# Optimization experiments

Hardware: AMD Instinct MI355X
Metric: run time of the kernel (lower is better)

## Reference

```python
import jax, jax.numpy as jnp
import numpy as np

HEADS = 12
LN_EPS = 1e-12
NUM_PROTOTYPES = 8


def _layer_norm(x, g, b):
    mu = x.mean(-1, keepdims=True)
    var = ((x - mu) ** 2).mean(-1, keepdims=True)
    return (x - mu) / jnp.sqrt(var + LN_EPS) * g + b


def _bert_attention(q_in, kv_in, wq, bq, wk, bk, wv, bv, wo, bo, ln_g, ln_b):
    # HF BertAttention: MHA (query from q_in, key/value from kv_in) then
    # SelfOutput: dense + residual(q_in) + LayerNorm. Dropout = 0 (eval).
    B, Sq, D = q_in.shape
    Sk = kv_in.shape[1]
    dh = D // HEADS
    q = (q_in @ wq + bq).reshape(B, Sq, HEADS, dh).transpose(0, 2, 1, 3)
    k = (kv_in @ wk + bk).reshape(B, Sk, HEADS, dh).transpose(0, 2, 1, 3)
    v = (kv_in @ wv + bv).reshape(B, Sk, HEADS, dh).transpose(0, 2, 1, 3)
    scores = jnp.einsum('bhqd,bhkd->bhqk', q, k) / jnp.sqrt(jnp.asarray(dh, q.dtype))
    probs = jax.nn.softmax(scores, axis=-1)
    ctx = jnp.einsum('bhqk,bhkd->bhqd', probs, v).transpose(0, 2, 1, 3).reshape(B, Sq, D)
    return _layer_norm(ctx @ wo + bo + q_in, ln_g, ln_b)


def setup_inputs() -> dict:
    key = jax.random.key(0)
    ks = jax.random.split(key, 16)
    D = 768
    inp = {
        'local_feats': jax.random.normal(ks[0], (8, 256, D), jnp.float32),
        'global_feat_dict': jax.random.normal(ks[1], (16384, D), jnp.float32),
    }
    i = 2
    for pre in ('ll', 'lg'):
        for nm in ('wq', 'wk', 'wv', 'wo'):
            inp[f'{pre}_{nm}'] = 0.02 * jax.random.normal(ks[i], (D, D), jnp.float32)
            i += 1
        for nm in ('bq', 'bk', 'bv', 'bo'):
            inp[f'{pre}_{nm}'] = jnp.zeros((D,), jnp.float32)
        inp[f'{pre}_ln_g'] = jnp.ones((D,), jnp.float32)
        inp[f'{pre}_ln_b'] = jnp.zeros((D,), jnp.float32)
    inp['ln_g'] = jnp.ones((D,), jnp.float32)
    inp['ln_b'] = jnp.zeros((D,), jnp.float32)
    inp['aug_w'] = 0.02 * jax.random.normal(ks[i], (D, 1), jnp.float32)
    inp['ori_w'] = 0.02 * jax.random.normal(ks[i + 1], (D, 1), jnp.float32)
    inp['aug_b'] = jnp.zeros((1,), jnp.float32)
    inp['ori_b'] = jnp.zeros((1,), jnp.float32)
    return inp


def reference(local_feats, global_feat_dict,
              ll_wq, ll_bq, ll_wk, ll_bk, ll_wv, ll_bv, ll_wo, ll_bo, ll_ln_g, ll_ln_b,
              lg_wq, lg_bq, lg_wk, lg_bk, lg_wv, lg_bv, lg_wo, lg_bo, lg_ln_g, lg_ln_b,
              ln_g, ln_b, aug_w, aug_b, ori_w, ori_b):
    B, L, D = local_feats.shape
    K = NUM_PROTOTYPES
    # similarity_topk retrieval: cosine similarity against prototype pool
    g_norm = global_feat_dict / jnp.linalg.norm(global_feat_dict, axis=-1, keepdims=True)
    t_norm = local_feats / jnp.linalg.norm(local_feats, axis=-1, keepdims=True)
    sim = jnp.einsum('bld,nd->bln', t_norm, g_norm)          # [B, L, N]
    topk_idx = jax.lax.top_k(sim, K)[1]                       # [B, L, K]
    global_feats = global_feat_dict[topk_idx].reshape(B, L * K, D)
    # self-attn over locals, cross-attn locals -> retrieved prototypes
    ll = _bert_attention(local_feats, local_feats,
                         ll_wq, ll_bq, ll_wk, ll_bk, ll_wv, ll_bv, ll_wo, ll_bo, ll_ln_g, ll_ln_b)
    lg = _bert_attention(local_feats, global_feats,
                         lg_wq, lg_bq, lg_wk, lg_bk, lg_wv, lg_bv, lg_wo, lg_bo, lg_ln_g, lg_ln_b)
    out = _layer_norm(ll + lg, ln_g, ln_b)
    aug_weight = jax.nn.sigmoid(out @ aug_w + aug_b + local_feats @ ori_w + ori_b)
    return aug_weight * out + (1.0 - aug_weight) * local_feats
```

## Files before the change

### kernel.cpp

```cpp
#include <hip/hip_runtime.h>
#include <math.h>

#define D     768
#define HEADS 12
#define DH    64
#define BATCH 8
#define LSEQ  256
#define MROWS 2048
#define NDICT 16384
#define TOPK  8

typedef _Float16 half_t;
typedef half_t half8 __attribute__((ext_vector_type(8)));
typedef float floatx4 __attribute__((ext_vector_type(4)));

#define F_DICT   0u
#define F_TN     6291456u
#define F_LOC    7077888u
#define F_WT     7864320u
#define F_BF     10223616u
#define F_TOPI   10231808u
#define F_LP     10248192u
#define F_SIM    13393920u
#define F_CTX    30171136u
#define F_D1     30957568u
#define F_CANDV  30957568u
#define F_CANDI  31088640u
#define F_ML     34103296u
#define F_NRM    34299904u
#define F_USED   34316288u
#define F_ROWMAP 34332672u
#define F_INVMAP 34349056u
#define F_CNT    34365440u

typedef const __attribute__((address_space(1))) void* gptr_as1;
typedef __attribute__((address_space(3))) void* lptr_as3;
#define GLDS16(gp, lp) __builtin_amdgcn_global_load_lds((gptr_as1)(gp), (lptr_as3)(lp), 16, 0, 0)

__device__ __forceinline__ float bsum(float v, float* red) {
  int t = threadIdx.x;
#pragma unroll
  for (int d = 32; d > 0; d >>= 1) v += __shfl_xor(v, d);
  if ((t & 63) == 0) red[t >> 6] = v;
  __syncthreads();
  float r = red[0] + red[1] + red[2] + red[3];
  __syncthreads();
  return r;
}

__global__ __launch_bounds__(256) void k_prep_wt(
    const float* __restrict__ dict, const float* __restrict__ local,
    half_t* __restrict__ gdict_h, float* __restrict__ dnrm,
    half_t* __restrict__ loc_h, half_t* __restrict__ tn_h,
    const float* w0, const float* w1, const float* w2, const float* w3,
    const float* w4, const float* w5, const float* w6, const float* w7,
    const float* b0, const float* b1, const float* b2, const float* b3,
    const float* b4, const float* b5, const float* b6, const float* b7,
    half_t* __restrict__ Wt, float* __restrict__ bfout) {
  __shared__ float red[8];
  __shared__ float tile[32][33];
  int g = blockIdx.x, t = threadIdx.x;
  if (g < NDICT) {
    const float* xr = dict + (size_t)g * D;
    float v0 = xr[t], v1 = xr[t + 256], v2 = xr[t + 512];
    float s = bsum(v0*v0 + v1*v1 + v2*v2, red);
    float n = sqrtf(s), inv = 1.0f / n;
    half_t* yr = gdict_h + (size_t)g * D;
    yr[t] = (half_t)(v0*inv); yr[t+256] = (half_t)(v1*inv); yr[t+512] = (half_t)(v2*inv);
    if (t == 0) dnrm[g] = n;
  } else if (g < NDICT + MROWS) {
    size_t r = g - NDICT;
    const float* xr = local + r * (size_t)D;
    float v0 = xr[t], v1 = xr[t + 256], v2 = xr[t + 512];
    float s = bsum(v0*v0 + v1*v1 + v2*v2, red);
    float inv = 1.0f / sqrtf(s);
    half_t* rr = loc_h + r * (size_t)D;
    half_t* nr = tn_h + r * (size_t)D;
    rr[t] = (half_t)v0;        rr[t+256] = (half_t)v1;        rr[t+512] = (half_t)v2;
    nr[t] = (half_t)(v0*inv);  nr[t+256] = (half_t)(v1*inv);  nr[t+512] = (half_t)(v2*inv);
  } else {
    const float* wsrcs[8] = {w0,w1,w2,w3,w4,w5,w6,w7};
    const float* bsrcs[8] = {b0,b1,b2,b3,b4,b5,b6,b7};
    int id = g - (NDICT + MROWS);
    int z = id / 576, rem = id % 576;
    int by = rem / 24, bx = rem % 24;
    const float* Wsrc = wsrcs[z];
    half_t* dst = Wt + (size_t)z * D * D;
    int tx = t & 31, ty = t >> 5;
    int c0 = bx * 32, r0 = by * 32;
#pragma unroll
    for (int j = 0; j < 4; j++)
      tile[ty + j*8][tx] = Wsrc[(size_t)(r0 + ty + j*8) * D + c0 + tx];
    __syncthreads();
#pragma unroll
    for (int j = 0; j < 4; j++)
      dst[(size_t)(c0 + ty + j*8) * D + r0 + tx] = (half_t)tile[tx][ty + j*8];
    if (bx == 0 && by == 0) {
#pragma unroll
      for (int j = 0; j < 3; j++)
        bfout[z * D + t + j*256] = bsrcs[z][t + j*256];
    }
  }
}

__device__ __forceinline__ void hgemm_core(
    const half_t* __restrict__ A, const half_t* __restrict__ B,
    const float* __restrict__ bias, const float* __restrict__ dnrm,
    const int* __restrict__ rowmap, void* __restrict__ Cout,
    int N, int K, int outHalf, int bx, int by, int mhalf,
    half_t* As, half_t* Bs) {
  int tid = threadIdx.x;
  int wid = tid >> 6, lane = tid & 63;
  int l16 = lane & 15, quad = lane >> 4;
  int n0 = bx * 128, m0 = by * 128;
  if (mhalf && m0 >= mhalf) { B += (size_t)D * D; if (bias) bias += D; }
  int wm = (wid & 1) * 64, wn = (wid >> 1) * 64;

  int r0  = tid >> 3;
  int cbg = (tid & 7) ^ (r0 & 7);
  const half_t* Aps[4];
#pragma unroll
  for (int i = 0; i < 4; i++) {
    int mm = m0 + r0 + 32*i;
    int mr = rowmap ? rowmap[mm] : mm;
    Aps[i] = A + (size_t)mr * K + cbg * 8;
  }
  const half_t* Bp = B + (size_t)(n0 + r0) * K + cbg * 8;

  floatx4 acc[4][4];
#pragma unroll
  for (int i = 0; i < 4; i++)
#pragma unroll
    for (int j = 0; j < 4; j++) { acc[i][j][0]=0.f; acc[i][j][1]=0.f; acc[i][j][2]=0.f; acc[i][j][3]=0.f; }

  for (int k0 = 0; k0 < K; k0 += 64) {
#pragma unroll
    for (int i = 0; i < 4; i++)
      GLDS16(Aps[i] + k0, As + ((size_t)i*256 + wid*64) * 8);
#pragma unroll
    for (int i = 0; i < 4; i++)
      GLDS16(Bp + k0 + (size_t)i * 32 * K, Bs + ((size_t)i*256 + wid*64) * 8);
    __syncthreads();
#pragma unroll
    for (int ks = 0; ks < 2; ks++) {
      half8 af[4], bf[4];
#pragma unroll
      for (int i = 0; i < 4; i++) {
        int row = wm + i*16 + l16;
        int cb = (quad + ks*4) ^ (row & 7);
        af[i] = *(const half8*)&As[row*64 + cb*8];
      }
#pragma unroll
      for (int j = 0; j < 4; j++) {
        int row = wn + j*16 + l16;
        int cb = (quad + ks*4) ^ (row & 7);
        bf[j] = *(const half8*)&Bs[row*64 + cb*8];
      }
#pragma unroll
      for (int i = 0; i < 4; i++)
#pragma unroll
        for (int j = 0; j < 4; j++)
          acc[i][j] = __builtin_amdgcn_mfma_f32_16x16x32_f16(af[i], bf[j], acc[i][j], 0, 0, 0);
    }
    __syncthreads();
  }

  float bcol[4];
#pragma unroll
  for (int j = 0; j < 4; j++) bcol[j] = bias ? bias[n0 + wn + j*16 + l16] : 0.f;
  if (outHalf) {
    half_t* C = (half_t*)Cout;
#pragma unroll
    for (int i = 0; i < 4; i++)
#pragma unroll
      for (int r = 0; r < 4; r++) {
        int grow = m0 + wm + i*16 + quad*4 + r;
        float sc = dnrm ? dnrm[rowmap ? rowmap[grow] : grow] : 1.0f;
#pragma unroll
        for (int j = 0; j < 4; j++)
          C[(size_t)grow * N + n0 + wn + j*16 + l16] = (half_t)(acc[i][j][r] * sc + bcol[j]);
      }
  } else {
    float* C = (float*)Cout;
#pragma unroll
    for (int i = 0; i < 4; i++)
#pragma unroll
      for (int r = 0; r < 4; r++) {
        int grow = m0 + wm + i*16 + quad*4 + r;
        float sc = dnrm ? dnrm[rowmap ? rowmap[grow] : grow] : 1.0f;
#pragma unroll
        for (int j = 0; j < 4; j++)
          C[(size_t)grow * N + n0 + wn + j*16 + l16] = acc[i][j][r] * sc + bcol[j];
      }
  }
}

__device__ __forceinline__ void hgemm256_core(
    const half_t* __restrict__ A, const half_t* __restrict__ B,
    const float* __restrict__ bias, const float* __restrict__ dnrm,
    const int* __restrict__ rowmap, half_t* __restrict__ C,
    int N, int K, int bx, int by,
    half_t* As0, half_t* As1, half_t* Bs0, half_t* Bs1) {
  const int tid = threadIdx.x;
  const int wid = tid >> 6, lane = tid & 63;
  const int l16 = lane & 15, quad = lane >> 4;
  const int m0 = by * 256, n0 = bx * 256;

  const int r0 = tid >> 3;
  const int cg = (tid & 7) ^ (r0 & 7);
  const half_t* Aps[4]; const half_t* Bps[4];
#pragma unroll
  for (int i = 0; i < 4; i++) {
    int mm = m0 + r0 + i * 64;
    int mr = rowmap ? rowmap[mm] : mm;
    Aps[i] = A + (size_t)mr * K + cg * 8;
    Bps[i] = B + (size_t)(n0 + r0 + i * 64) * K + cg * 8;
  }

  const int arow = (wid & 3) * 32 + l16;
  const int brow = (wid >> 2) * 64 + l16;
  const int cb0 = (quad ^ (l16 & 7)) * 8;
  const int cb1 = ((quad + 4) ^ (l16 & 7)) * 8;

  floatx4 acc[4][2][4];
#pragma unroll
  for (int q = 0; q < 4; q++)
#pragma unroll
    for (int mi = 0; mi < 2; mi++)
#pragma unroll
      for (int ni = 0; ni < 4; ni++) {
        acc[q][mi][ni][0] = 0.f; acc[q][mi][ni][1] = 0.f;
        acc[q][mi][ni][2] = 0.f; acc[q][mi][ni][3] = 0.f;
      }
  half8 af[2][2], bf[4][2];

#define STAGE(Adst, Bdst, kn) { \
    GLDS16(Aps[0] + (kn), (Adst) + (0*512 + wid*64) * 8); \
    GLDS16(Aps[1] + (kn), (Adst) + (1*512 + wid*64) * 8); \
    GLDS16(Aps[2] + (kn), (Adst) + (2*512 + wid*64) * 8); \
    GLDS16(Aps[3] + (kn), (Adst) + (3*512 + wid*64) * 8); \
    GLDS16(Bps[0] + (kn), (Bdst) + (0*512 + wid*64) * 8); \
    GLDS16(Bps[1] + (kn), (Bdst) + (1*512 + wid*64) * 8); \
    GLDS16(Bps[2] + (kn), (Bdst) + (2*512 + wid*64) * 8); \
    GLDS16(Bps[3] + (kn), (Bdst) + (3*512 + wid*64) * 8); }
#define LDA(qm) { const int rb_ = (qm)*8192 + arow*64; \
    af[0][0] = *(const half8*)&Ar[rb_ + cb0];        af[0][1] = *(const half8*)&Ar[rb_ + cb1]; \
    af[1][0] = *(const half8*)&Ar[rb_ + 1024 + cb0]; af[1][1] = *(const half8*)&Ar[rb_ + 1024 + cb1]; }
#define LDB(qn) { const int rb_ = (qn)*8192 + brow*64; \
    bf[0][0] = *(const half8*)&Br[rb_ + cb0];        bf[0][1] = *(const half8*)&Br[rb_ + cb1]; \
    bf[1][0] = *(const half8*)&Br[rb_ + 1024 + cb0]; bf[1][1] = *(const half8*)&Br[rb_ + 1024 + cb1]; \
    bf[2][0] = *(const half8*)&Br[rb_ + 2048 + cb0]; bf[2][1] = *(const half8*)&Br[rb_ + 2048 + cb1]; \
    bf[3][0] = *(const half8*)&Br[rb_ + 3072 + cb0]; bf[3][1] = *(const half8*)&Br[rb_ + 3072 + cb1]; }
#define MM(q) { _Pragma("unroll") for (int mi = 0; mi < 2; mi++) { \
    _Pragma("unroll") for (int ni = 0; ni < 4; ni++) { \
      acc[q][mi][ni] = __builtin_amdgcn_mfma_f32_16x16x32_f16(af[mi][0], bf[ni][0], acc[q][mi][ni], 0, 0, 0); \
      acc[q][mi][ni] = __builtin_amdgcn_mfma_f32_16x16x32_f16(af[mi][1], bf[ni][1], acc[q][mi][ni], 0, 0, 0); } } }

  const int NT = K >> 6;
  STAGE(As0, Bs0, 0);
  __syncthreads();

  half_t* Ar = As0; half_t* Aw = As1;
  half_t* Br = Bs0; half_t* Bw = Bs1;
  for (int t = 0; t < NT; ++t) {
    if (t + 1 < NT) STAGE(Aw, Bw, (t + 1) * 64);
    LDA(0); LDB(0); MM(0);
    LDB(1);         MM(1);
    LDA(1);         MM(2);
    LDB(0);         MM(3);
    if (t + 1 < NT) __syncthreads();
    half_t* tp = Ar; Ar = Aw; Aw = tp;
    tp = Br; Br = Bw; Bw = tp;
  }

  float bcol[2][4];
#pragma unroll
  for (int qn = 0; qn < 2; qn++)
#pragma unroll
    for (int ni = 0; ni < 4; ni++)
      bcol[qn][ni] = bias ? bias[n0 + qn*128 + (wid >> 2)*64 + ni*16 + l16] : 0.f;
#pragma unroll
  for (int q = 0; q < 4; q++) {
    const int qm = q >> 1;
    const int qn = (q == 1 || q == 2) ? 1 : 0;
#pragma unroll
    for (int mi = 0; mi < 2; mi++)
#pragma unroll
      for (int r = 0; r < 4; r++) {
        int grow = m0 + qm*128 + (wid & 3)*32 + mi*16 + quad*4 + r;
        float sc = dnrm ? dnrm[rowmap ? rowmap[grow] : grow] : 1.0f;
#pragma unroll
        for (int ni = 0; ni < 4; ni++)
          C[(size_t)grow * N + n0 + qn*128 + (wid >> 2)*64 + ni*16 + l16] =
              (half_t)(acc[q][mi][ni][r] * sc + bcol[qn][ni]);
      }
  }
#undef STAGE
#undef LDA
#undef LDB
#undef MM
}

__global__ __launch_bounds__(512) void k_gemm_simlp(
    const half_t* __restrict__ tn, const half_t* __restrict__ gd,
    half_t* __restrict__ sim,
    const half_t* __restrict__ loc, const half_t* __restrict__ wt0,
    const float* __restrict__ bf0, half_t* __restrict__ lp) {
  __shared__ half_t As[2][256*64];
  __shared__ half_t Bs[2][256*64];
  int gid = blockIdx.x;
  int swz = (gid & 7) * 76 + (gid >> 3);
  if (swz < 512) {
    int bx = (swz & 7) + ((swz >> 3) >> 3) * 8;
    int by = (swz >> 3) & 7;
    hgemm256_core(tn, gd, nullptr, nullptr, nullptr, sim, NDICT, D, bx, by,
                  As[0], As[1], Bs[0], Bs[1]);
  } else {
    int rel = swz - 512;
    int bx = rel >> 3;
    int by = rel & 7;
    hgemm256_core(loc, wt0, bf0, nullptr, nullptr, lp, 3072, D, bx, by,
                  As[0], As[1], Bs[0], Bs[1]);
  }
}

__global__ __launch_bounds__(512) void k_gemm_dkv(
    const half_t* __restrict__ gd, const half_t* __restrict__ wt4,
    const float* __restrict__ bf4, const float* __restrict__ dnrm,
    const int* __restrict__ rowmap, const int* __restrict__ cnt,
    half_t* __restrict__ dkv) {
  __shared__ half_t As[2][256*64];
  __shared__ half_t Bs[2][256*64];
  int mceil = (*cnt + 255) & ~255;
  if ((int)blockIdx.y * 256 >= mceil) return;
  hgemm256_core(gd, wt4, bf4, dnrm, rowmap, dkv, 1536, D,
                blockIdx.x, blockIdx.y, As[0], As[1], Bs[0], Bs[1]);
}

__global__ __launch_bounds__(256) void k_gemm_wo(
    const half_t* __restrict__ ctx, const half_t* __restrict__ wt6,
    const float* __restrict__ bf6, float* __restrict__ dd) {
  __shared__ half_t As[128*64];
  __shared__ half_t Bs[128*64];
  hgemm_core(ctx, wt6, bf6, nullptr, nullptr, dd, D, D, 0, blockIdx.x, blockIdx.y, MROWS, As, Bs);
}

__global__ __launch_bounds__(256) void k_topk1(const half_t* __restrict__ sim,
                                               float* __restrict__ candv,
                                               int* __restrict__ candi,
                                               int* __restrict__ used,
                                               int* __restrict__ rowmap,
                                               int* __restrict__ cnt) {
  int t = threadIdx.x;
  if (t < 4) used[blockIdx.x * 4 + t] = 0;
  else if (t < 8) rowmap[blockIdx.x * 4 + t - 4] = 0;
  if (blockIdx.x == 0 && t == 8) *cnt = 0;

  int gw = blockIdx.x * 4 + (t >> 6);
  int lane = t & 63;
  int row = gw >> 3, seg = gw & 7;
  int cbase = seg * 2048;
  const half_t* p = sim + (size_t)row * NDICT + cbase;

  float v[32];
#pragma unroll
  for (int i = 0; i < 4; i++) {
    half8 h = *(const half8*)(p + i*512 + lane*8);
#pragma unroll
    for (int j = 0; j < 8; j++) v[i*8 + j] = (float)h[j];
  }
  float m = v[0]; int pos = 0;
#pragma unroll
  for (int i = 1; i < 32; i++) { if (v[i] > m) { m = v[i]; pos = i; } }

  for (int it = 0; it < 8; it++) {
    int gidx = cbase + (pos >> 3) * 512 + lane * 8 + (pos & 7);
    float bv = m; int bi = gidx;
#pragma unroll
    for (int d2 = 1; d2 < 64; d2 <<= 1) {
      float ov = __shfl_xor(bv, d2); int oi = __shfl_xor(bi, d2);
      if (ov > bv || (ov == bv && oi < bi)) { bv = ov; bi = oi; }
    }
    if (lane == 0) {
      size_t base = (size_t)row * 64 + seg * 8 + it;
      candv[base] = bv; candi[base] = bi;
    }
    if (bi == gidx) {
      v[pos] = -INFINITY;
      m = v[0]; pos = 0;
#pragma unroll
      for (int i = 1; i < 32; i++) { if (v[i] > m) { m = v[i]; pos = i; } }
    }
  }
}

__global__ __launch_bounds__(256) void k_topk2(const float* __restrict__ candv,
                                               const int* __restrict__ candi,
                                               int* __restrict__ topi,
                                               int* __restrict__ used) {
  int row = blockIdx.x * 4 + (threadIdx.x >> 6);
  int lane = threadIdx.x & 63;
  float v = candv[(size_t)row * 64 + lane];
  int id = candi[(size_t)row * 64 + lane];
#pragma unroll
  for (int it = 0; it < 8; it++) {
    float bv = v; int bi = id;
#pragma unroll
    for (int d2 = 1; d2 < 64; d2 <<= 1) {
      float ov = __shfl_xor(bv, d2); int oi = __shfl_xor(bi, d2);
      if (ov > bv || (ov == bv && oi < bi)) { bv = ov; bi = oi; }
    }
    if (lane == 0) { topi[row * 8 + it] = bi; used[bi] = 1; }
    if (id == bi) { v = -INFINITY; id = 0x7FFFFFFF; }
  }
}

__global__ __launch_bounds__(256) void k_cmp(const int* __restrict__ used,
                                             int* __restrict__ rowmap,
                                             int* __restrict__ invmap,
                                             int* __restrict__ cnt) {
  int i = blockIdx.x * 256 + threadIdx.x;
  if (used[i]) { int s = atomicAdd(cnt, 1); rowmap[s] = i; invmap[i] = s; }
}
__global__ __launch_bounds__(256) void k_remap(int* __restrict__ topi,
                                               const int* __restrict__ invmap) {
  int i = blockIdx.x * 256 + threadIdx.x;
  topi[i] = invmap[topi[i]];
}

__global__ __launch_bounds__(256) void k_flash2(
    const half_t* __restrict__ lp, const half_t* __restrict__ dkv,
    const int* __restrict__ topi_,
    half_t* __restrict__ ctx_ll, half_t* __restrict__ Opart, float* __restrict__ ml) {
  __shared__ half_t Ks[64][72];
  __shared__ half_t Vt[64][72];
  __shared__ half_t Ps[4][16][72];

  int tid = threadIdx.x;
  int wid = tid >> 6;
  int lane = tid & 63;
  int l16 = lane & 15, quad = lane >> 4;

  const half_t *Q, *K, *V; const int* kidx; half_t* Out;
  int qS, kvS, Sk, ns, rel;
  if (blockIdx.x < BATCH*HEADS*4*4) {
    rel = blockIdx.x;
    Q = lp + 2304; qS = 3072; K = dkv; V = dkv + 768; kvS = 1536;
    kidx = topi_; Sk = LSEQ*TOPK; ns = 4; Out = nullptr;
  } else {
    rel = blockIdx.x - BATCH*HEADS*4*4;
    Q = lp; qS = 3072; K = lp + 768; V = lp + 1536; kvS = 3072;
    kidx = nullptr; Sk = LSEQ; ns = 1; Out = ctx_ll;
  }

  int sp = rel % ns;
  int rest = rel / ns;
  int qt = rest & 3;
  int h  = (rest >> 2) % HEADS;
  int bb = rest / (4 * HEADS);
  int q0 = qt * 64 + wid * 16;
  int sLen = Sk / ns, s0 = sp * sLen;

  const float SCL = 0.125f * 1.4426950408889634f;
  const half_t* qrow = Q + (size_t)(bb * LSEQ + q0 + l16) * qS + h * DH;
  half8 aq0 = *(const half8*)(qrow + quad*8);
  half8 aq1 = *(const half8*)(qrow + 32 + quad*8);

  floatx4 o[4];
#pragma unroll
  for (int nt = 0; nt < 4; nt++) { o[nt][0]=0.f; o[nt][1]=0.f; o[nt][2]=0.f; o[nt][3]=0.f; }
  float mreg[4] = {-INFINITY, -INFINITY, -INFINITY, -INFINITY};
  float lreg[4] = {0.f, 0.f, 0.f, 0.f};

  for (int k0 = s0; k0 < s0 + sLen; k0 += 64) {
    {
      int row = tid >> 2, cg = tid & 3;
      int key = k0 + row;
      size_t rowid = kidx ? (size_t)kidx[(size_t)bb * Sk + key]
                          : (size_t)(bb * LSEQ + key);
      const half_t* kb = K + rowid * (size_t)kvS + h * DH + cg * 16;
      const half_t* vb = V + rowid * (size_t)kvS + h * DH + cg * 16;
      *(half8*)&Ks[row][cg*16]     = *(const half8*)kb;
      *(half8*)&Ks[row][cg*16 + 8] = *(const half8*)(kb + 8);
      half8 v0 = *(const half8*)vb, v1 = *(const half8*)(vb + 8);
#pragma unroll
      for (int jj = 0; jj < 8; jj++) { Vt[cg*16 + jj][row] = v0[jj]; Vt[cg*16 + 8 + jj][row] = v1[jj]; }
    }
    __syncthreads();

    floatx4 c[4];
#pragma unroll
    for (int nt = 0; nt < 4; nt++) {
      half8 b0 = *(const half8*)&Ks[nt*16 + l16][quad*8];
      half8 b1 = *(const half8*)&Ks[nt*16 + l16][32 + quad*8];
      floatx4 z; z[0]=0.f; z[1]=0.f; z[2]=0.f; z[3]=0.f;
      z = __builtin_amdgcn_mfma_f32_16x16x32_f16(aq0, b0, z, 0, 0, 0);
      z = __builtin_amdgcn_mfma_f32_16x16x32_f16(aq1, b1, z, 0, 0, 0);
      c[nt] = z;
    }

    float alpha[4];
#pragma unroll
    for (int r = 0; r < 4; r++) {
      float mx = fmaxf(fmaxf(c[0][r], c[1][r]), fmaxf(c[2][r], c[3][r]));
      mx = fmaxf(mx, __shfl_xor(mx, 1));
      mx = fmaxf(mx, __shfl_xor(mx, 2));
      mx = fmaxf(mx, __shfl_xor(mx, 4));
      mx = fmaxf(mx, __shfl_xor(mx, 8));
      float mn = fmaxf(mreg[r], mx);
      float al = __builtin_amdgcn_exp2f((mreg[r] - mn) * SCL);
      float ps = 0.f;
#pragma unroll
      for (int nt = 0; nt < 4; nt++) {
        float p = __builtin_amdgcn_exp2f((c[nt][r] - mn) * SCL);
        c[nt][r] = p; ps += p;
      }
      ps += __shfl_xor(ps, 1);
      ps += __shfl_xor(ps, 2);
      ps += __shfl_xor(ps, 4);
      ps += __shfl_xor(ps, 8);
      mreg[r] = mn; lreg[r] = lreg[r] * al + ps; alpha[r] = al;
    }

#pragma unroll
    for (int nt = 0; nt < 4; nt++)
#pragma unroll
      for (int r = 0; r < 4; r++)
        Ps[wid][quad*4 + r][nt*16 + l16] = (half_t)c[nt][r];
    half8 p0 = *(const half8*)&Ps[wid][l16][quad*8];
    half8 p1 = *(const half8*)&Ps[wid][l16][32 + quad*8];

#pragma unroll
    for (int nt = 0; nt < 4; nt++)
#pragma unroll
      for (int r = 0; r < 4; r++) o[nt][r] *= alpha[r];
#pragma unroll
    for (int nt = 0; nt < 4; nt++) {
      half8 v0 = *(const half8*)&Vt[nt*16 + l16][quad*8];
      half8 v1 = *(const half8*)&Vt[nt*16 + l16][32 + quad*8];
      o[nt] = __builtin_amdgcn_mfma_f32_16x16x32_f16(p0, v0, o[nt], 0, 0, 0);
      o[nt] = __builtin_amdgcn_mfma_f32_16x16x32_f16(p1, v1, o[nt], 0, 0, 0);
    }
    __syncthreads();
  }

  if (ns == 1) {
    half_t* ob = Out + (size_t)(bb * LSEQ + q0 + quad*4) * D + h * DH;
#pragma unroll
    for (int r = 0; r < 4; r++) {
      float inv = 1.0f / lreg[r];
#pragma unroll
      for (int nt = 0; nt < 4; nt++)
        ob[(size_t)r * D + nt*16 + l16] = (half_t)(o[nt][r] * inv);
    }
  } else {
    size_t rbase = (size_t)sp * MROWS + bb * LSEQ + q0 + quad*4;
    half_t* ob = Opart + rbase * D + h * DH;
#pragma unroll
    for (int r = 0; r < 4; r++) {
      float inv = 1.0f / lreg[r];
#pragma unroll
      for (int nt = 0; nt < 4; nt++)
        ob[(size_t)r * D + nt*16 + l16] = (half_t)(o[nt][r] * inv);
    }
    if (l16 == 0) {
#pragma unroll
      for (int r = 0; r < 4; r++) {
        size_t mi = ((rbase + r) * HEADS + h) * 2;
        ml[mi] = mreg[r]; ml[mi + 1] = lreg[r];
      }
    }
  }
}

__global__ __launch_bounds__(256) void k_comb(const half_t* __restrict__ Op,
                                              const float* __restrict__ ml,
                                              half_t* __restrict__ ctx) {
  int r = blockIdx.x, t = threadIdx.x;
  const float SCL = 0.125f * 1.4426950408889634f;
#pragma unroll
  for (int i = 0; i < 3; i++) {
    int col = t + i*256;
    int h = col >> 6;
    float m[4], l[4];
    float ms = -INFINITY;
#pragma unroll
    for (int s = 0; s < 4; s++) {
      size_t mi = (((size_t)s * MROWS + r) * HEADS + h) * 2;
      m[s] = ml[mi]; l[s] = ml[mi + 1];
      ms = fmaxf(ms, m[s]);
    }
    float den = 0.f, num = 0.f;
#pragma unroll
    for (int s = 0; s < 4; s++) {
      float w = __builtin_amdgcn_exp2f((m[s] - ms) * SCL) * l[s];
      den += w;
      num += w * (float)Op[((size_t)s * MROWS + r) * D + col];
    }
    ctx[(size_t)r * D + col] = (half_t)(num / den);
  }
}

__global__ __launch_bounds__(256) void k_lngate3(
    const float* __restrict__ dd, const float* __restrict__ loc,
    const float* __restrict__ llg, const float* __restrict__ llb,
    const float* __restrict__ lgg, const float* __restrict__ lgb,
    const float* __restrict__ lng, const float* __restrict__ lnb,
    const float* __restrict__ aw, const float* __restrict__ ow,
    const float* __restrict__ ab, const float* __restrict__ orb,
    float* __restrict__ y) {
  __shared__ float red[8];
  size_t r = blockIdx.x; int t = threadIdx.x;
  const float* ar = dd + r*(size_t)D;
  const float* br = dd + ((size_t)MROWS + r)*(size_t)D;
  const float* lcl = loc + r*(size_t)D;
  float l0 = lcl[t], l1 = lcl[t+256], l2 = lcl[t+512];

  float a0 = ar[t]+l0, a1 = ar[t+256]+l1, a2 = ar[t+512]+l2;
  float mu = bsum(a0+a1+a2, red) * (1.0f/768.0f);
  float d0 = a0-mu, d1 = a1-mu, d2 = a2-mu;
  float var = bsum(d0*d0 + d1*d1 + d2*d2, red) * (1.0f/768.0f);
  float rstd = rsqrtf(var + 1e-12f);
  float x0 = d0*rstd*llg[t]     + llb[t];
  float x1 = d1*rstd*llg[t+256] + llb[t+256];
  float x2 = d2*rstd*llg[t+512] + llb[t+512];

  float b0 = br[t]+l0, b1 = br[t+256]+l1, b2 = br[t+512]+l2;
  mu = bsum(b0+b1+b2, red) * (1.0f/768.0f);
  d0 = b0-mu; d1 = b1-mu; d2 = b2-mu;
  var = bsum(d0*d0 + d1*d1 + d2*d2, red) * (1.0f/768.0f);
  rstd = rsqrtf(var + 1e-12f);
  x0 += d0*rstd*lgg[t]     + lgb[t];
  x1 += d1*rstd*lgg[t+256] + lgb[t+256];
  x2 += d2*rstd*lgg[t+512] + lgb[t+512];

  mu = bsum(x0+x1+x2, red) * (1.0f/768.0f);
  d0 = x0-mu; d1 = x1-mu; d2 = x2-mu;
  var = bsum(d0*d0 + d1*d1 + d2*d2, red) * (1.0f/768.0f);
  rstd = rsqrtf(var + 1e-12f);
  float o0 = d0*rstd*lng[t]     + lnb[t];
  float o1 = d1*rstd*lng[t+256] + lnb[t+256];
  float o2 = d2*rstd*lng[t+512] + lnb[t+512];

  float s = o0*aw[t] + l0*ow[t]
          + o1*aw[t+256] + l1*ow[t+256]
          + o2*aw[t+512] + l2*ow[t+512];
  float z = bsum(s, red) + ab[0] + orb[0];
  float w = 1.0f / (1.0f + __expf(-z));
  float* yr = y + r*(size_t)D;
  yr[t]     = w*o0 + (1.f-w)*l0;
  yr[t+256] = w*o1 + (1.f-w)*l1;
  yr[t+512] = w*o2 + (1.f-w)*l2;
}

extern "C" void kernel_launch(void* const* d_in, const int* in_sizes, int n_in,
                              void* d_out, int out_size, void* d_ws, size_t ws_size,
                              hipStream_t stream) {
  (void)in_sizes; (void)n_in; (void)out_size; (void)ws_size;
  const float* local = (const float*)d_in[0];
  const float* dict  = (const float*)d_in[1];
  const float* ll_g  = (const float*)d_in[10];
  const float* ll_b  = (const float*)d_in[11];
  const float* lg_g  = (const float*)d_in[20];
  const float* lg_b  = (const float*)d_in[21];
  const float* ln_g  = (const float*)d_in[22];
  const float* ln_b  = (const float*)d_in[23];
  const float* aug_w = (const float*)d_in[24];
  const float* ori_w = (const float*)d_in[25];
  const float* aug_b = (const float*)d_in[26];
  const float* ori_b = (const float*)d_in[27];

  float* W = (float*)d_ws;
  half_t* gdict_h = (half_t*)(W + F_DICT);
  half_t* tn_h    = (half_t*)(W + F_TN);
  half_t* loc_h   = (half_t*)(W + F_LOC);
  half_t* wt      = (half_t*)(W + F_WT);
  float*  bf      = W + F_BF;
  int*    topi    = (int*)(W + F_TOPI);
  half_t* lp      = (half_t*)(W + F_LP);
  half_t* sim_h   = (half_t*)(W + F_SIM);
  half_t* dkv     = (half_t*)(W + F_SIM);
  float*  dd      = W + F_SIM;
  half_t* ctx_ll  = (half_t*)(W + F_CTX);
  half_t* ctx_lg  = (half_t*)(W + F_D1);
  half_t* Opart   = (half_t*)(W + F_D1);
  float*  candv   = W + F_CANDV;
  int*    candi   = (int*)(W + F_CANDI);
  float*  ml      = W + F_ML;
  float*  dnrm    = W + F_NRM;
  int*    used    = (int*)(W + F_USED);
  int*    rowmap  = (int*)(W + F_ROWMAP);
  int*    invmap  = (int*)(W + F_INVMAP);
  int*    cnt     = (int*)(W + F_CNT);

  dim3 blk(256);
  dim3 blk5(512);
  const size_t WS = (size_t)D * D;

  k_prep_wt<<<NDICT + MROWS + 4608, blk, 0, stream>>>(
      dict, local, gdict_h, dnrm, loc_h, tn_h,
      (const float*)d_in[2], (const float*)d_in[3], (const float*)d_in[4],
      (const float*)d_in[12], (const float*)d_in[13], (const float*)d_in[14],
      (const float*)d_in[5], (const float*)d_in[15],
      (const float*)d_in[6], (const float*)d_in[7], (const float*)d_in[8],
      (const float*)d_in[16], (const float*)d_in[17], (const float*)d_in[18],
      (const float*)d_in[9], (const float*)d_in[19], wt, bf);

  k_gemm_simlp<<<512 + 96, blk5, 0, stream>>>(tn_h, gdict_h, sim_h,
                                              loc_h, wt + 0*WS, bf + 0, lp);

  k_topk1<<<MROWS*8/4, blk, 0, stream>>>(sim_h, candv, candi, used, rowmap, cnt);
  k_topk2<<<MROWS/4, blk, 0, stream>>>(candv, candi, topi, used);
  k_cmp<<<64, blk, 0, stream>>>(used, rowmap, invmap, cnt);
  k_remap<<<64, blk, 0, stream>>>(topi, invmap);

  k_gemm_dkv<<<dim3(6, 64), blk5, 0, stream>>>(
      gdict_h, wt + 4*WS, bf + 3072, dnrm, rowmap, cnt, dkv);

  k_flash2<<<dim3(BATCH*HEADS*4*4 + BATCH*HEADS*4), blk, 0, stream>>>(
      lp, dkv, topi, ctx_ll, Opart, ml);
  k_comb<<<MROWS, blk, 0, stream>>>(Opart, ml, ctx_lg);

  k_gemm_wo<<<dim3(6, 32), blk, 0, stream>>>(ctx_ll, wt + 6*WS, bf + 4608, dd);

  k_lngate3<<<MROWS, blk, 0, stream>>>(dd, local,
      ll_g, ll_b, lg_g, lg_b, ln_g, ln_b,
      aug_w, ori_w, aug_b, ori_b, (float*)d_out);
}
```

Before: 428.5 us.

## Interleave global-to-LDS staging with MFMA quadrants using fine-grained waitcnt and barriers

Restructures the 256x256 hgemm main loop so the next tile's global-to-LDS loads are issued in pieces between the four MFMA quadrant phases instead of all at once. It uses explicit vmcnt waits, raw s_barriers, sched_barriers, and s_setprio around the MFMA blocks, with a peeled final iteration. The goal is to overlap memory traffic with compute and keep the waves in lockstep. The extra barriers add synchronisation cost, and the hand-placed waitcnt values must match the load ordering exactly or the kernel will read stale LDS.

```diff
diff --git a/kernel.cpp b/kernel.cpp
--- a/kernel.cpp
+++ b/kernel.cpp
@@ -234,15 +234,8 @@
       }
   half8 af[2][2], bf[4][2];
 
-#define STAGE(Adst, Bdst, kn) { \
-    GLDS16(Aps[0] + (kn), (Adst) + (0*512 + wid*64) * 8); \
-    GLDS16(Aps[1] + (kn), (Adst) + (1*512 + wid*64) * 8); \
-    GLDS16(Aps[2] + (kn), (Adst) + (2*512 + wid*64) * 8); \
-    GLDS16(Aps[3] + (kn), (Adst) + (3*512 + wid*64) * 8); \
-    GLDS16(Bps[0] + (kn), (Bdst) + (0*512 + wid*64) * 8); \
-    GLDS16(Bps[1] + (kn), (Bdst) + (1*512 + wid*64) * 8); \
-    GLDS16(Bps[2] + (kn), (Bdst) + (2*512 + wid*64) * 8); \
-    GLDS16(Bps[3] + (kn), (Bdst) + (3*512 + wid*64) * 8); }
+#define STG_A(dst, i, kn) GLDS16(Aps[i] + (kn), (dst) + ((i)*512 + wid*64) * 8)
+#define STG_B(dst, i, kn) GLDS16(Bps[i] + (kn), (dst) + ((i)*512 + wid*64) * 8)
 #define LDA(qm) { const int rb_ = (qm)*8192 + arow*64; \
     af[0][0] = *(const half8*)&Ar[rb_ + cb0];        af[0][1] = *(const half8*)&Ar[rb_ + cb1]; \
     af[1][0] = *(const half8*)&Ar[rb_ + 1024 + cb0]; af[1][1] = *(const half8*)&Ar[rb_ + 1024 + cb1]; }
@@ -255,23 +248,67 @@
     _Pragma("unroll") for (int ni = 0; ni < 4; ni++) { \
       acc[q][mi][ni] = __builtin_amdgcn_mfma_f32_16x16x32_f16(af[mi][0], bf[ni][0], acc[q][mi][ni], 0, 0, 0); \
       acc[q][mi][ni] = __builtin_amdgcn_mfma_f32_16x16x32_f16(af[mi][1], bf[ni][1], acc[q][mi][ni], 0, 0, 0); } } }
-
-  const int NT = K >> 6;
-  STAGE(As0, Bs0, 0);
-  __syncthreads();
+#define VMC(n) asm volatile("s_waitcnt vmcnt(" #n ")" ::: "memory")
+#define SBAR() __builtin_amdgcn_s_barrier()
+#define SCHED0() __builtin_amdgcn_sched_barrier(0)
+
+  STG_A(As0, 0, 0); STG_A(As0, 1, 0);
+  STG_B(Bs0, 0, 0); STG_B(Bs0, 1, 0);
+  STG_B(Bs0, 2, 0); STG_B(Bs0, 3, 0);
+  STG_A(As0, 2, 0); STG_A(As0, 3, 0);
+  VMC(4); SBAR();
 
   half_t* Ar = As0; half_t* Aw = As1;
   half_t* Br = Bs0; half_t* Bw = Bs1;
-  for (int t = 0; t < NT; ++t) {
-    if (t + 1 < NT) STAGE(Aw, Bw, (t + 1) * 64);
-    LDA(0); LDB(0); MM(0);
-    LDB(1);         MM(1);
-    LDA(1);         MM(2);
-    LDB(0);         MM(3);
-    if (t + 1 < NT) __syncthreads();
+
+  const int NT = K >> 6;
+  for (int t = 0; t < NT - 1; ++t) {
+    const int kn = (t + 1) * 64;
+    SCHED0();
+    LDA(0); LDB(0);
+    STG_A(Aw, 0, kn); STG_A(Aw, 1, kn);
+    VMC(4); SBAR(); SCHED0();
+    __builtin_amdgcn_s_setprio(1); MM(0); __builtin_amdgcn_s_setprio(0);
+    SBAR();
+    SCHED0();
+    LDB(1);
+    STG_B(Bw, 0, kn); STG_B(Bw, 1, kn);
+    VMC(4); SBAR(); SCHED0();
+    __builtin_amdgcn_s_setprio(1); MM(1); __builtin_amdgcn_s_setprio(0);
+    SBAR();
+    SCHED0();
+    LDA(1);
+    STG_B(Bw, 2, kn); STG_B(Bw, 3, kn);
+    SBAR(); SCHED0();
+    __builtin_amdgcn_s_setprio(1); MM(2); __builtin_amdgcn_s_setprio(0);
+    SBAR();
+    SCHED0();
+    LDB(0);
+    STG_A(Aw, 2, kn); STG_A(Aw, 3, kn);
+    VMC(4); SBAR(); SCHED0();
+    __builtin_amdgcn_s_setprio(1); MM(3); __builtin_amdgcn_s_setprio(0);
+    SBAR();
     half_t* tp = Ar; Ar = Aw; Aw = tp;
     tp = Br; Br = Bw; Bw = tp;
   }
+  SCHED0();
+  LDA(0); LDB(0);
+  VMC(2); SBAR(); SCHED0();
+  __builtin_amdgcn_s_setprio(1); MM(0); __builtin_amdgcn_s_setprio(0);
+  SBAR();
+  SCHED0();
+  LDB(1);
+  VMC(0); SBAR(); SCHED0();
+  __builtin_amdgcn_s_setprio(1); MM(1); __builtin_amdgcn_s_setprio(0);
+  SBAR();
+  SCHED0();
+  LDA(1);
+  SBAR(); SCHED0();
+  __builtin_amdgcn_s_setprio(1); MM(2); __builtin_amdgcn_s_setprio(0);
+  SBAR();
+  SCHED0();
+  LDB(0);
+  __builtin_amdgcn_s_setprio(1); MM(3); __builtin_amdgcn_s_setprio(0);
 
   float bcol[2][4];
 #pragma unroll
@@ -295,10 +332,14 @@
               (half_t)(acc[q][mi][ni][r] * sc + bcol[qn][ni]);
       }
   }
-#undef STAGE
+#undef STG_A
+#undef STG_B
 #undef LDA
 #undef LDB
 #undef MM
+#undef VMC
+#undef SBAR
+#undef SCHED0
 }
 
 __global__ __launch_bounds__(512) void k_gemm_simlp(
```

Result: no change. 431.4 us (+0.7%).
